# Performance work log

Hardware: AMD Instinct MI355X
Metric: run time of the kernel (lower is better)

## Reference

```python
import jax, jax.numpy as jnp
import numpy as np

N, E, F, R, L, B = 50000, 800000, 64, 20, 2, 64
RC = 5.0
ZMAX = 100
LN2 = 0.6931471805599453

def ssp(x):
    # shifted softplus: softplus(x) - log(2)
    return jax.nn.softplus(x) - LN2

def setup_inputs() -> dict:
    key = jax.random.key(0)
    ks = jax.random.split(key, 32)
    w = lambda i, shape: jax.random.normal(ks[i], shape, dtype=jnp.float32) * 0.05
    inp = {
        'z': jax.random.randint(ks[0], (N,), 0, ZMAX + 1),
        'pos': jax.random.normal(ks[1], (N, 3), dtype=jnp.float32) * 3.0,
        'edge_index': jax.random.randint(ks[2], (2, E), 0, N),
        'batch_idx': jnp.sort(jax.random.randint(ks[3], (N,), 0, B)),
        'emb': jax.random.normal(ks[4], (ZMAX + 1, F), dtype=jnp.float32),
        'phi_W': w(5, (L, 3 * F, F)), 'phi_b': w(6, (L, 3 * F)),
        'filt_W1': w(7, (L, F, R)), 'filt_b1': w(8, (L, F)),
        'filt_W2': w(9, (L, 3 * F, F)), 'filt_b2': w(10, (L, 3 * F)),
        'U_W': w(11, (L, F, F)), 'V_W': w(12, (L, F, F)),
        'a_W1': w(13, (L, F, 2 * F)), 'a_b1': w(14, (L, F)),
        'a_W2': w(15, (L, 3 * F, F)), 'a_b2': w(16, (L, 3 * F)),
        'e_W1': w(17, (F // 2, F)), 'e_b1': w(18, (F // 2,)),
        'e_W2': w(19, (1, F // 2)), 'e_b2': w(20, (1,)),
        'dip_w': w(21, (F,)),
    }
    return inp

def reference(z, pos, edge_index, batch_idx, emb, phi_W, phi_b,
              filt_W1, filt_b1, filt_W2, filt_b2, U_W, V_W,
              a_W1, a_b1, a_W2, a_b2, e_W1, e_b1, e_W2, e_b2, dip_w):
    src, dst = edge_index[0], edge_index[1]
    s = emb[z]                               # (N, F)
    v = jnp.zeros((N, F, 3), dtype=s.dtype)  # (N, F, 3)

    # edge geometry
    r_vec = pos[dst] - pos[src]              # (E, 3)
    r_norm = jnp.linalg.norm(r_vec, axis=-1)
    r_hat = r_vec / jnp.maximum(r_norm, 1e-8)[:, None]
    # Gaussian RBF on [0, RC], widths = grid spacing
    mu = jnp.linspace(0.0, RC, R, dtype=s.dtype)
    width = mu[1] - mu[0]
    e_ij = jnp.exp(-((r_norm[:, None] - mu[None, :]) ** 2) / (2.0 * width * width))
    fc = 0.5 * (jnp.cos(jnp.pi * r_norm / RC) + 1.0) * (r_norm < RC)
    e_ij = e_ij * fc[:, None]                # (E, R)

    for l in range(L):
        # message block
        filt = ssp(e_ij @ filt_W1[l].T + filt_b1[l]) @ filt_W2[l].T + filt_b2[l]  # (E, 3F)
        W_s, W_v, W_r = jnp.split(filt, 3, axis=-1)
        phi = s[dst] @ phi_W[l].T + phi_b[l]                                       # (E, 3F)
        phi_s, phi_v, phi_r = jnp.split(phi, 3, axis=-1)
        m_s = W_s * phi_s                                                          # (E, F)
        m_v = W_v[:, :, None] * v[dst] + (W_r * phi_r)[:, :, None] * r_hat[:, None, :]  # (E, F, 3)
        s = s + jax.ops.segment_sum(m_s, src, num_segments=N)
        v = v + jax.ops.segment_sum(m_v, src, num_segments=N)
        # update block
        Uv = jnp.einsum('nfd,gf->ngd', v, U_W[l])
        Vv = jnp.einsum('nfd,gf->ngd', v, V_W[l])
        Vv_norm_sq = jnp.sum(Vv * Vv, axis=-1)                                     # (N, F)
        a = ssp(jnp.concatenate([s, Vv_norm_sq], axis=-1) @ a_W1[l].T + a_b1[l]) @ a_W2[l].T + a_b2[l]
        a_ss, a_sv, a_vv = jnp.split(a, 3, axis=-1)
        inner = jnp.sum(Uv * Vv, axis=-1)
        s = s + a_ss + a_sv * inner
        v = v + a_vv[:, :, None] * Uv

    # heads
    eps_i = (ssp(s @ e_W1.T + e_b1) @ e_W2.T + e_b2)[:, 0]  # (N,)
    energy = jax.ops.segment_sum(eps_i, batch_idx, num_segments=B)
    mu_i = jnp.sum(v * dip_w[None, :, None], axis=1)         # (N, 3)
    mu_mol = jax.ops.segment_sum(mu_i, batch_idx, num_segments=B)
    dipole = jnp.linalg.norm(mu_mol, axis=-1)
    charges = jnp.zeros((N,), dtype=s.dtype)
    return energy, dipole, charges
```

## Files before the change

kernel.cpp:

```cpp
#include <hip/hip_runtime.h>
#include <math.h>

static constexpr int N  = 50000;
static constexpr int E  = 800000;
static constexpr int F  = 64;
static constexpr int R  = 20;
static constexpr int NL = 2;
static constexpr int B  = 64;
static constexpr float RC   = 5.0f;
static constexpr float LN2F = 0.6931471805599453f;
static constexpr float WIDTH  = RC / (R - 1);
static constexpr float INV2W2 = 1.0f / (2.0f * WIDTH * WIDTH);
static constexpr float PI_F = 3.14159265358979323846f;

static constexpr int   NB     = 4096;
static constexpr float DR     = RC / NB;
static constexpr float INV_DR = NB / RC;
static constexpr int   TROWS  = NB + 2;
static constexpr int   TENT   = NB + 1;

static constexpr int NBLK_SCAN = (N + 255) / 256;

typedef __attribute__((ext_vector_type(8))) short bf16x8;
typedef __attribute__((ext_vector_type(4))) float f32x4;
typedef __attribute__((ext_vector_type(3))) unsigned uint32x3;

__device__ __forceinline__ float ssp_f(float x) {
    return fmaxf(x, 0.0f) + log1pf(__expf(-fabsf(x))) - LN2F;
}

__device__ __forceinline__ short f2bf(float x) {
    unsigned u = __builtin_bit_cast(unsigned, x);
    unsigned r = (u + 0x7fffu + ((u >> 16) & 1u)) >> 16;
    return (short)r;
}
__device__ __forceinline__ float bf_lo(unsigned u) {
    return __builtin_bit_cast(float, u << 16);
}
__device__ __forceinline__ float bf_hi(unsigned u) {
    return __builtin_bit_cast(float, u & 0xffff0000u);
}

__global__ void k_hist(const int* __restrict__ ei, int* __restrict__ cnt) {
    int e = blockIdx.x * blockDim.x + threadIdx.x;
    if (e < E) atomicAdd(&cnt[ei[e]], 1);
}

__global__ void k_scan_a(const int* __restrict__ cnt, int* __restrict__ bsum) {
    __shared__ int part[256];
    const int t = threadIdx.x;
    const int idx = blockIdx.x * 256 + t;
    int v = (idx < N) ? cnt[idx] : 0;
    part[t] = v;
    __syncthreads();
    for (int d = 1; d < 256; d <<= 1) {
        int x = (t >= d) ? part[t - d] : 0;
        __syncthreads();
        part[t] += x;
        __syncthreads();
    }
    if (t == 255) bsum[blockIdx.x] = part[255];
}

__global__ void k_scan_b(const int* __restrict__ bsum, int* __restrict__ bpre,
                         int* __restrict__ offN) {
    __shared__ int part[256];
    const int t = threadIdx.x;
    int v = (t < NBLK_SCAN) ? bsum[t] : 0;
    part[t] = v;
    __syncthreads();
    for (int d = 1; d < 256; d <<= 1) {
        int x = (t >= d) ? part[t - d] : 0;
        __syncthreads();
        part[t] += x;
        __syncthreads();
    }
    if (t < NBLK_SCAN) bpre[t] = part[t] - v;
    if (t == NBLK_SCAN - 1) *offN = part[t];
}

__global__ void k_scan_c(const int* __restrict__ cnt, const int* __restrict__ bpre,
                         int* __restrict__ off, int* __restrict__ curN,
                         int* __restrict__ curF) {
    __shared__ int part[256];
    const int t = threadIdx.x;
    const int idx = blockIdx.x * 256 + t;
    int v = (idx < N) ? cnt[idx] : 0;
    part[t] = v;
    __syncthreads();
    for (int d = 1; d < 256; d <<= 1) {
        int x = (t >= d) ? part[t - d] : 0;
        __syncthreads();
        part[t] += x;
        __syncthreads();
    }
    if (idx < N) {
        int e = bpre[blockIdx.x] + part[t] - v;
        off[idx] = e;
        curN[idx] = e;
        curF[idx] = e + v;
    }
}

__global__ void k_scatter(const int* __restrict__ ei, int* __restrict__ curN,
                          int* __restrict__ curF,
                          const float* __restrict__ pos, uint4* __restrict__ edata) {
    int e = blockIdx.x * blockDim.x + threadIdx.x;
    if (e >= E) return;
    int src = ei[e], dst = ei[E + e];
    float qx = pos[dst * 3 + 0] - pos[src * 3 + 0];
    float qy = pos[dst * 3 + 1] - pos[src * 3 + 1];
    float qz = pos[dst * 3 + 2] - pos[src * 3 + 2];
    float rn = sqrtf(qx * qx + qy * qy + qz * qz);
    float invn = 1.0f / fmaxf(rn, 1e-8f);
    float t = rn * INV_DR;
    int i = (int)t;
    float fr = t - (float)i;
    const bool far = (i >= NB);
    if (far) { i = NB; fr = 0.0f; }
    int p = far ? (atomicAdd(&curF[src], -1) - 1) : atomicAdd(&curN[src], 1);
    uint4 rec;
    rec.x = (unsigned)dst;
    rec.y = (unsigned)i | ((unsigned)(unsigned short)f2bf(fr) << 16);
    rec.z = (unsigned)(unsigned short)f2bf(qx * invn)
          | ((unsigned)(unsigned short)f2bf(qy * invn) << 16);
    rec.w = (unsigned)(unsigned short)f2bf(qz * invn);
    edata[p] = rec;
}

__global__ void k_table(const float* __restrict__ fW1, const float* __restrict__ fb1,
                        const float* __restrict__ fW2, const float* __restrict__ fb2,
                        unsigned short* __restrict__ Tp) {
    const int l   = blockIdx.x / TROWS;
    const int row = blockIdx.x % TROWS;
    const int lane = threadIdx.x;
    const float r = fminf((float)row, (float)NB) * DR;
    const float fc = (r < RC) ? 0.5f * (__cosf(PI_F * r * (1.0f / RC)) + 1.0f) : 0.0f;

    __shared__ float sh[F];
    float acc = fb1[l * F + lane];
    const float* w1 = fW1 + (size_t)l * F * R + (size_t)lane * R;
    #pragma unroll
    for (int rr = 0; rr < R; rr++) {
        float dmu = r - rr * WIDTH;
        float er = __expf(-dmu * dmu * INV2W2) * fc;
        acc = fmaf(er, w1[rr], acc);
    }
    sh[lane] = ssp_f(acc);
    __syncthreads();
    unsigned short* TpL = Tp + (size_t)l * TENT * 384;
    #pragma unroll
    for (int p = 0; p < 3; p++) {
        int c = p * 64 + lane;
        float a = fb2[l * 192 + c];
        const float* w2 = fW2 + ((size_t)l * 192 + c) * 64;
        #pragma unroll 8
        for (int k = 0; k < F; k++) a = fmaf(sh[k], w2[k], a);
        unsigned short bf = (unsigned short)f2bf(a);
        if (row <= NB) TpL[(size_t)row * 384 + lane * 6 + p * 2 + 0] = bf;
        if (row >= 1)  TpL[(size_t)(row - 1) * 384 + lane * 6 + p * 2 + 1] = bf;
    }
}

__launch_bounds__(256)
__global__ void k_pack0(float* __restrict__ s, const int* __restrict__ z,
                        const float* __restrict__ emb,
                        const float* __restrict__ PW, const float* __restrict__ Pb,
                        unsigned* __restrict__ ndA) {
    __shared__ float sbuf[4][F];
    const int lane = threadIdx.x & 63;
    const int wid  = threadIdx.x >> 6;
    const int gwave = blockIdx.x * 4 + wid;
    const int nwaves = gridDim.x * 4;

    float wsr[F], wrr[F];
    {
        const float* rs = PW + (size_t)lane * 64;
        const float* rr = PW + (size_t)(128 + lane) * 64;
        #pragma unroll
        for (int k = 0; k < F; k += 4) {
            float4 a = *(const float4*)(rs + k);
            wsr[k] = a.x; wsr[k+1] = a.y; wsr[k+2] = a.z; wsr[k+3] = a.w;
            float4 b = *(const float4*)(rr + k);
            wrr[k] = b.x; wrr[k+1] = b.y; wrr[k+2] = b.z; wrr[k+3] = b.w;
        }
    }
    const float bs = Pb[lane], br = Pb[128 + lane];

    for (int n = gwave; n < N; n += nwaves) {
        float sv = emb[(size_t)z[n] * F + lane];
        s[(size_t)n * F + lane] = sv;
        sbuf[wid][lane] = sv;
        float as = bs, ar = br;
        #pragma unroll
        for (int k = 0; k < F; k += 4) {
            float4 s4 = *(const float4*)&sbuf[wid][k];
            as = fmaf(s4.x, wsr[k],   as); as = fmaf(s4.y, wsr[k+1], as);
            as = fmaf(s4.z, wsr[k+2], as); as = fmaf(s4.w, wsr[k+3], as);
            ar = fmaf(s4.x, wrr[k],   ar); ar = fmaf(s4.y, wrr[k+1], ar);
            ar = fmaf(s4.z, wrr[k+2], ar); ar = fmaf(s4.w, wrr[k+3], ar);
        }
        ndA[(size_t)n * 64 + lane] = (unsigned)(unsigned short)f2bf(as)
                                   | ((unsigned)(unsigned short)f2bf(ar) << 16);
    }
}

template<bool ACCUMV>
__launch_bounds__(256, 8)
__global__ void k_gather(const uint4* __restrict__ edata, const int* __restrict__ off,
                         const int* __restrict__ mid,
                         const unsigned short* __restrict__ TpL,
                         const unsigned* __restrict__ ndA, const uint2* __restrict__ ndV,
                         float* __restrict__ s, float* __restrict__ v) {
    __shared__ float red[4][4][64];
    const int lane = threadIdx.x & 63;
    const int wv   = threadIdx.x >> 6;
    const int n = blockIdx.x;
    const int base = off[n], m = mid[n], end = off[n + 1];

    float ms = 0.f, mv0 = 0.f, mv1 = 0.f, mv2 = 0.f;

    for (int k = base + wv; k < m; k += 4) {
        const uint4 ed = edata[k];
        const int i = (int)(ed.y & 0xffffu);
        const uint32x3 t = *(const uint32x3*)(TpL + (size_t)i * 384 + lane * 6);
        const unsigned a = ndA[(size_t)ed.x * 64 + lane];
        const float fr = bf_hi(ed.y);
        const float Ws = fmaf(fr, bf_hi(t.x) - bf_lo(t.x), bf_lo(t.x));
        const float Wr = fmaf(fr, bf_hi(t.z) - bf_lo(t.z), bf_lo(t.z));
        ms = fmaf(Ws, bf_lo(a), ms);
        const float c = Wr * bf_hi(a);
        const float rhx = bf_lo(ed.z), rhy = bf_hi(ed.z), rhz = bf_lo(ed.w);
        if (ACCUMV) {
            const float Wv = fmaf(fr, bf_hi(t.y) - bf_lo(t.y), bf_lo(t.y));
            const uint2 w = ndV[(size_t)ed.x * 64 + lane];
            mv0 = fmaf(Wv, bf_lo(w.x), fmaf(c, rhx, mv0));
            mv1 = fmaf(Wv, bf_hi(w.x), fmaf(c, rhy, mv1));
            mv2 = fmaf(Wv, bf_lo(w.y), fmaf(c, rhz, mv2));
        } else {
            mv0 = fmaf(c, rhx, mv0);
            mv1 = fmaf(c, rhy, mv1);
            mv2 = fmaf(c, rhz, mv2);
        }
    }

    {
        const uint32x3 tF = *(const uint32x3*)(TpL + (size_t)NB * 384 + lane * 6);
        const float WsF = bf_lo(tF.x), WvF = bf_lo(tF.y), WrF = bf_lo(tF.z);
        int kc = m + wv;
        if (kc < end) {
            uint4 edC = edata[kc];
            int kn = kc + 4;
            bool hasN = kn < end;
            uint4 edN = edC;
            if (hasN) edN = edata[kn];
            unsigned aC = ndA[(size_t)edC.x * 64 + lane];
            uint2 wC = {0, 0};
            if (ACCUMV) wC = ndV[(size_t)edC.x * 64 + lane];
            for (;;) {
                const int kn2 = kn + 4;
                const bool hasN2 = hasN && (kn2 < end);
                uint4 edN2 = edC;
                if (hasN2) edN2 = edata[kn2];
                unsigned aN = aC;
                uint2 wN = wC;
                if (hasN) {
                    aN = ndA[(size_t)edN.x * 64 + lane];
                    if (ACCUMV) wN = ndV[(size_t)edN.x * 64 + lane];
                }
                ms = fmaf(WsF, bf_lo(aC), ms);
                const float c = WrF * bf_hi(aC);
                const float rhx = bf_lo(edC.z), rhy = bf_hi(edC.z), rhz = bf_lo(edC.w);
                if (ACCUMV) {
                    mv0 = fmaf(WvF, bf_lo(wC.x), fmaf(c, rhx, mv0));
                    mv1 = fmaf(WvF, bf_hi(wC.x), fmaf(c, rhy, mv1));
                    mv2 = fmaf(WvF, bf_lo(wC.y), fmaf(c, rhz, mv2));
                } else {
                    mv0 = fmaf(c, rhx, mv0);
                    mv1 = fmaf(c, rhy, mv1);
                    mv2 = fmaf(c, rhz, mv2);
                }
                if (!hasN) break;
                edC = edN; aC = aN; wC = wN;
                edN = edN2; hasN = hasN2; kn = kn2;
            }
        }
    }

    red[wv][0][lane] = ms;
    red[wv][1][lane] = mv0;
    red[wv][2][lane] = mv1;
    red[wv][3][lane] = mv2;
    __syncthreads();
    if (wv == 0) {
        ms  = red[0][0][lane] + red[1][0][lane] + red[2][0][lane] + red[3][0][lane];
        mv0 = red[0][1][lane] + red[1][1][lane] + red[2][1][lane] + red[3][1][lane];
        mv1 = red[0][2][lane] + red[1][2][lane] + red[2][2][lane] + red[3][2][lane];
        mv2 = red[0][3][lane] + red[1][3][lane] + red[2][3][lane] + red[3][3][lane];
        s[(size_t)n * F + lane] += ms;
        float* vo = v + (size_t)n * 3 * F + lane;
        if (ACCUMV) {
            vo[0]     += mv0;
            vo[F]     += mv1;
            vo[2 * F] += mv2;
        } else {
            vo[0] = mv0; vo[F] = mv1; vo[2 * F] = mv2;
        }
    }
}

__device__ __forceinline__ bf16x8 load_wfrag(const float* __restrict__ Wp, int ldk,
                                             int nrow, int k0) {
    const float* p = Wp + (size_t)nrow * ldk + k0;
    float4 a = *(const float4*)p;
    float4 b = *(const float4*)(p + 4);
    bf16x8 r;
    r[0] = f2bf(a.x); r[1] = f2bf(a.y); r[2] = f2bf(a.z); r[3] = f2bf(a.w);
    r[4] = f2bf(b.x); r[5] = f2bf(b.y); r[6] = f2bf(b.z); r[7] = f2bf(b.w);
    return r;
}

template<bool DO_PACK>
__launch_bounds__(256)
__global__ void k_update_mfma(float* __restrict__ s, float* __restrict__ v,
                              const float* __restrict__ U_W, const float* __restrict__ V_W,
                              const float* __restrict__ aW1, const float* __restrict__ ab1,
                              const float* __restrict__ aW2, const float* __restrict__ ab2,
                              const float* __restrict__ PW, const float* __restrict__ Pb,
                              unsigned* __restrict__ ndA, uint2* __restrict__ ndV) {
    __shared__ short vlds[96 * 72];
    __shared__ short xlds[32 * 136];
    __shared__ short hlds[32 * 72];

    const int tid = threadIdx.x;
    const int l   = tid & 63;
    const int w   = tid >> 6;
    const int lo  = l & 15;
    const int hi  = l >> 4;

    bf16x8 ufr[2], vfr[2], w1fr[4], w2fr[3][2];
    #pragma unroll
    for (int kk = 0; kk < 2; kk++) {
        ufr[kk] = load_wfrag(U_W, 64, w * 16 + lo, kk * 32 + hi * 8);
        vfr[kk] = load_wfrag(V_W, 64, w * 16 + lo, kk * 32 + hi * 8);
    }
    #pragma unroll
    for (int kk = 0; kk < 4; kk++)
        w1fr[kk] = load_wfrag(aW1, 128, w * 16 + lo, kk * 32 + hi * 8);
    #pragma unroll
    for (int p = 0; p < 3; p++)
        #pragma unroll
        for (int kk = 0; kk < 2; kk++)
            w2fr[p][kk] = load_wfrag(aW2, 64, p * 64 + w * 16 + lo, kk * 32 + hi * 8);

    bf16x8 pws[2], pwr[2];
    float pbs = 0.f, pbr = 0.f;
    if (DO_PACK) {
        #pragma unroll
        for (int kk = 0; kk < 2; kk++) {
            pws[kk] = load_wfrag(PW, 64, w * 16 + lo, kk * 32 + hi * 8);
            pwr[kk] = load_wfrag(PW, 64, 128 + w * 16 + lo, kk * 32 + hi * 8);
        }
        pbs = Pb[w * 16 + lo];
        pbr = Pb[128 + w * 16 + lo];
    }

    const float ab1c  = ab1[w * 16 + lo];
    const float ab2c0 = ab2[w * 16 + lo];
    const float ab2c1 = ab2[64 + w * 16 + lo];
    const float ab2c2 = ab2[128 + w * 16 + lo];
    const int g = w * 16 + lo;

    for (int half = 0; half < 2; half++) {
        const int n0 = blockIdx.x * 64 + half * 32;
        if (half) __syncthreads();

        for (int u = tid; u < 96 * 8; u += 256) {
            int row = u >> 3, oct = u & 7;
            int d = row >> 5, nn = row & 31;
            int n = min(n0 + nn, N - 1);
            const float* src = v + ((size_t)n * 3 + d) * 64 + oct * 8;
            float4 a = *(const float4*)src;
            float4 b = *(const float4*)(src + 4);
            bf16x8 t;
            t[0] = f2bf(a.x); t[1] = f2bf(a.y); t[2] = f2bf(a.z); t[3] = f2bf(a.w);
            t[4] = f2bf(b.x); t[5] = f2bf(b.y); t[6] = f2bf(b.z); t[7] = f2bf(b.w);
            *(bf16x8*)&vlds[row * 72 + oct * 8] = t;
        }
        for (int u = tid; u < 32 * 8; u += 256) {
            int nn = u >> 3, oct = u & 7;
            int n = min(n0 + nn, N - 1);
            const float* src = s + (size_t)n * 64 + oct * 8;
            float4 a = *(const float4*)src;
            float4 b = *(const float4*)(src + 4);
            bf16x8 t;
            t[0] = f2bf(a.x); t[1] = f2bf(a.y); t[2] = f2bf(a.z); t[3] = f2bf(a.w);
            t[4] = f2bf(b.x); t[5] = f2bf(b.y); t[6] = f2bf(b.z); t[7] = f2bf(b.w);
            *(bf16x8*)&xlds[nn * 136 + oct * 8] = t;
        }
        __syncthreads();

        f32x4 cu[6], cv[6];
        #pragma unroll
        for (int mt = 0; mt < 6; mt++) { cu[mt] = (f32x4)0.0f; cv[mt] = (f32x4)0.0f; }
        #pragma unroll
        for (int kk = 0; kk < 2; kk++) {
            #pragma unroll
            for (int mt = 0; mt < 6; mt++) {
                bf16x8 af = *(const bf16x8*)&vlds[(mt * 16 + lo) * 72 + kk * 32 + hi * 8];
                cu[mt] = __builtin_amdgcn_mfma_f32_16x16x32_bf16(af, ufr[kk], cu[mt], 0, 0, 0);
                cv[mt] = __builtin_amdgcn_mfma_f32_16x16x32_bf16(af, vfr[kk], cv[mt], 0, 0, 0);
            }
        }

        f32x4 inn[2];
        #pragma unroll
        for (int nt = 0; nt < 2; nt++) {
            #pragma unroll
            for (int r = 0; r < 4; r++) {
                float vs = 0.f, ii = 0.f;
                #pragma unroll
                for (int d = 0; d < 3; d++) {
                    float a = cu[d * 2 + nt][r], b = cv[d * 2 + nt][r];
                    vs = fmaf(b, b, vs);
                    ii = fmaf(a, b, ii);
                }
                inn[nt][r] = ii;
                int nl = nt * 16 + hi * 4 + r;
                xlds[nl * 136 + 64 + w * 16 + lo] = f2bf(vs);
            }
        }
        __syncthreads();

        f32x4 c2[2];
        c2[0] = (f32x4)0.0f; c2[1] = (f32x4)0.0f;
        #pragma unroll
        for (int kk = 0; kk < 4; kk++) {
            #pragma unroll
            for (int mt = 0; mt < 2; mt++) {
                bf16x8 af = *(const bf16x8*)&xlds[(mt * 16 + lo) * 136 + kk * 32 + hi * 8];
                c2[mt] = __builtin_amdgcn_mfma_f32_16x16x32_bf16(af, w1fr[kk], c2[mt], 0, 0, 0);
            }
        }
        #pragma unroll
        for (int mt = 0; mt < 2; mt++)
            #pragma unroll
            for (int r = 0; r < 4; r++) {
                float hv = ssp_f(c2[mt][r] + ab1c);
                hlds[(mt * 16 + hi * 4 + r) * 72 + w * 16 + lo] = f2bf(hv);
            }
        __syncthreads();

        f32x4 c3[2][3];
        #pragma unroll
        for (int mt = 0; mt < 2; mt++)
            #pragma unroll
            for (int p = 0; p < 3; p++) c3[mt][p] = (f32x4)0.0f;
        #pragma unroll
        for (int kk = 0; kk < 2; kk++) {
            #pragma unroll
            for (int mt = 0; mt < 2; mt++) {
                bf16x8 af = *(const bf16x8*)&hlds[(mt * 16 + lo) * 72 + kk * 32 + hi * 8];
                #pragma unroll
                for (int p = 0; p < 3; p++)
                    c3[mt][p] = __builtin_amdgcn_mfma_f32_16x16x32_bf16(af, w2fr[p][kk], c3[mt][p], 0, 0, 0);
            }
        }

        float snew[2][4];
        #pragma unroll
        for (int mt = 0; mt < 2; mt++) {
            #pragma unroll
            for (int r = 0; r < 4; r++) {
                int n = n0 + mt * 16 + hi * 4 + r;
                if (n >= N) { snew[mt][r] = 0.f; continue; }
                float a_ss = c3[mt][0][r] + ab2c0;
                float a_sv = c3[mt][1][r] + ab2c1;
                float a_vv = c3[mt][2][r] + ab2c2;
                size_t si = (size_t)n * 64 + g;
                float sn = s[si] + a_ss + a_sv * inn[mt][r];
                s[si] = sn;
                snew[mt][r] = sn;
                float vn[3];
                #pragma unroll
                for (int d = 0; d < 3; d++) {
                    size_t vi = ((size_t)n * 3 + d) * 64 + g;
                    vn[d] = v[vi] + a_vv * cu[d * 2 + mt][r];
                    v[vi] = vn[d];
                }
                if (DO_PACK) {
                    uint2 pv;
                    pv.x = (unsigned)(unsigned short)f2bf(vn[0])
                         | ((unsigned)(unsigned short)f2bf(vn[1]) << 16);
                    pv.y = (unsigned)(unsigned short)f2bf(vn[2]);
                    ndV[(size_t)n * 64 + g] = pv;
                }
            }
        }

        if (DO_PACK) {
            __syncthreads();
            #pragma unroll
            for (int mt = 0; mt < 2; mt++)
                #pragma unroll
                for (int r = 0; r < 4; r++)
                    hlds[(mt * 16 + hi * 4 + r) * 72 + g] = f2bf(snew[mt][r]);
            __syncthreads();

            f32x4 cs[2], cr[2];
            cs[0] = (f32x4)0.0f; cs[1] = (f32x4)0.0f;
            cr[0] = (f32x4)0.0f; cr[1] = (f32x4)0.0f;
            #pragma unroll
            for (int kk = 0; kk < 2; kk++) {
                #pragma unroll
                for (int mt = 0; mt < 2; mt++) {
                    bf16x8 af = *(const bf16x8*)&hlds[(mt * 16 + lo) * 72 + kk * 32 + hi * 8];
                    cs[mt] = __builtin_amdgcn_mfma_f32_16x16x32_bf16(af, pws[kk], cs[mt], 0, 0, 0);
                    cr[mt] = __builtin_amdgcn_mfma_f32_16x16x32_bf16(af, pwr[kk], cr[mt], 0, 0, 0);
                }
            }
            #pragma unroll
            for (int mt = 0; mt < 2; mt++) {
                #pragma unroll
                for (int r = 0; r < 4; r++) {
                    int n = n0 + mt * 16 + hi * 4 + r;
                    if (n >= N) continue;
                    ndA[(size_t)n * 64 + g] =
                          (unsigned)(unsigned short)f2bf(cs[mt][r] + pbs)
                        | ((unsigned)(unsigned short)f2bf(cr[mt][r] + pbr) << 16);
                }
            }
        }
    }
}

__global__ void k_heads(const float* __restrict__ s, const float* __restrict__ v,
                        const int* __restrict__ batch_idx,
                        const float* __restrict__ eW1, const float* __restrict__ eb1,
                        const float* __restrict__ eW2, const float* __restrict__ eb2,
                        const float* __restrict__ dip_w,
                        float* __restrict__ eacc, float* __restrict__ macc) {
    __shared__ float se[B];
    __shared__ float sm[3][B];
    if (threadIdx.x < B) se[threadIdx.x] = 0.0f;
    if (threadIdx.x < 3 * B) sm[threadIdx.x >> 6][threadIdx.x & 63] = 0.0f;
    __syncthreads();
    int n = blockIdx.x * blockDim.x + threadIdx.x;
    if (n < N) {
        int b = batch_idx[n];
        float sr[F];
        #pragma unroll
        for (int f = 0; f < F; f += 4) {
            float4 t = *(const float4*)&s[(size_t)n * F + f];
            sr[f] = t.x; sr[f+1] = t.y; sr[f+2] = t.z; sr[f+3] = t.w;
        }
        float eps = eb2[0];
        for (int jj = 0; jj < F / 2; jj++) {
            float acc = eb1[jj];
            #pragma unroll
            for (int f = 0; f < F; f++)
                acc = fmaf(sr[f], eW1[jj * F + f], acc);
            eps = fmaf(eW2[jj], ssp_f(acc), eps);
        }
        atomicAdd(&se[b], eps);
        #pragma unroll
        for (int d = 0; d < 3; d++) {
            float m = 0.0f;
            #pragma unroll 8
            for (int f = 0; f < F; f++)
                m = fmaf(v[((size_t)n * 3 + d) * F + f], dip_w[f], m);
            atomicAdd(&sm[d][b], m);
        }
    }
    __syncthreads();
    if (threadIdx.x < B) atomicAdd(&eacc[threadIdx.x], se[threadIdx.x]);
    if (threadIdx.x >= B && threadIdx.x < 4 * B) {
        int d = (threadIdx.x >> 6) - 1, b = threadIdx.x & 63;
        atomicAdd(&macc[d * B + b], sm[d][b]);
    }
}

__global__ void k_final(const float* __restrict__ eacc, const float* __restrict__ macc,
                        float* __restrict__ out) {
    int b = threadIdx.x;
    if (b < B) {
        out[b] = eacc[b];
        float mx = macc[b], my = macc[B + b], mz = macc[2 * B + b];
        out[B + b] = sqrtf(mx * mx + my * my + mz * mz);
    }
}

extern "C" void kernel_launch(void* const* d_in, const int* in_sizes, int n_in,
                              void* d_out, int out_size, void* d_ws, size_t ws_size,
                              hipStream_t stream) {
    const int*   z     = (const int*)d_in[0];
    const float* pos   = (const float*)d_in[1];
    const int*   ei    = (const int*)d_in[2];
    const int*   bidx  = (const int*)d_in[3];
    const float* emb   = (const float*)d_in[4];
    const float* phi_W = (const float*)d_in[5];
    const float* phi_b = (const float*)d_in[6];
    const float* fW1   = (const float*)d_in[7];
    const float* fb1   = (const float*)d_in[8];
    const float* fW2   = (const float*)d_in[9];
    const float* fb2   = (const float*)d_in[10];
    const float* U_W   = (const float*)d_in[11];
    const float* V_W   = (const float*)d_in[12];
    const float* aW1   = (const float*)d_in[13];
    const float* ab1   = (const float*)d_in[14];
    const float* aW2   = (const float*)d_in[15];
    const float* ab2   = (const float*)d_in[16];
    const float* eW1   = (const float*)d_in[17];
    const float* eb1   = (const float*)d_in[18];
    const float* eW2   = (const float*)d_in[19];
    const float* eb2   = (const float*)d_in[20];
    const float* dip_w = (const float*)d_in[21];
    float* out = (float*)d_out;

    float* ws = (float*)d_ws;
    float* s    = ws;
    float* v    = s + (size_t)N * F;
    unsigned* ndA = (unsigned*)(v + (size_t)N * F * 3);
    uint2* ndV  = (uint2*)(ndA + (size_t)N * 64);
    unsigned short* Tp = (unsigned short*)(ndV + (size_t)N * 64);
    float* eacc = (float*)(Tp + (size_t)NL * TENT * 384);
    float* macc = eacc + B;
    int*   cnt  = (int*)(macc + 3 * B);
    int*   off  = cnt  + N;
    int*   curN = off  + N + 1;
    int*   curF = curN + N;
    int*   bsum = curF + N;
    int*   bpre = bsum + 256;
    uint4* edata = (uint4*)(((uintptr_t)(bpre + 256) + 15) & ~(uintptr_t)15);

    hipMemsetAsync(cnt,  0, sizeof(int) * N, stream);
    hipMemsetAsync(eacc, 0, sizeof(float) * 4 * B, stream);
    hipMemsetAsync(out + 2 * B, 0, sizeof(float) * (size_t)N, stream);

    k_hist<<<(E + 255) / 256, 256, 0, stream>>>(ei, cnt);
    k_scan_a<<<NBLK_SCAN, 256, 0, stream>>>(cnt, bsum);
    k_scan_b<<<1, 256, 0, stream>>>(bsum, bpre, off + N);
    k_scan_c<<<NBLK_SCAN, 256, 0, stream>>>(cnt, bpre, off, curN, curF);
    k_scatter<<<(E + 255) / 256, 256, 0, stream>>>(ei, curN, curF, pos, edata);
    k_table<<<NL * TROWS, 64, 0, stream>>>(fW1, fb1, fW2, fb2, Tp);

    const int ublocks = (N + 63) / 64;
    k_pack0<<<512, 256, 0, stream>>>(s, z, emb, phi_W, phi_b, ndA);
    k_gather<false><<<N, 256, 0, stream>>>(edata, off, curN, Tp, ndA, ndV, s, v);
    k_update_mfma<true><<<ublocks, 256, 0, stream>>>(s, v,
        U_W, V_W, aW1, ab1, aW2, ab2,
        phi_W + (size_t)192 * 64, phi_b + 192, ndA, ndV);
    k_gather<true><<<N, 256, 0, stream>>>(edata, off, curN,
        Tp + (size_t)TENT * 384, ndA, ndV, s, v);
    k_update_mfma<false><<<ublocks, 256, 0, stream>>>(s, v,
        U_W + 4096, V_W + 4096, aW1 + 8192, ab1 + F, aW2 + 12288, ab2 + 192,
        nullptr, nullptr, nullptr, nullptr);

    k_heads<<<(N + 255) / 256, 256, 0, stream>>>(s, v, bidx, eW1, eb1, eW2, eb2,
                                                 dip_w, eacc, macc);
    k_final<<<1, 64, 0, stream>>>(eacc, macc, out);
}
```

Measured before the change: 527.9 us.

## Assign one wave per node in gather and interleave node A/V packs

The gather kernel now maps each node to a single wave, four nodes per block, instead of splitting one node's edges across four waves. This removes the shared-memory reduction and the block barrier. The loop now handles near and far edges in one software-pipelined loop that prefetches the table row. The separate ndA and ndV node arrays are merged into one 12-byte-per-lane interleaved array, so the second-layer gather issues a single 12-byte load per neighbor instead of two loads. High-degree nodes now run serially on one wave, which may raise per-node latency and cause load imbalance.

```diff
diff --git a/kernel.cpp b/kernel.cpp
--- a/kernel.cpp
+++ b/kernel.cpp
@@ -166,7 +166,7 @@
 __global__ void k_pack0(float* __restrict__ s, const int* __restrict__ z,
                         const float* __restrict__ emb,
                         const float* __restrict__ PW, const float* __restrict__ Pb,
-                        unsigned* __restrict__ ndA) {
+                        unsigned* __restrict__ ndA0) {
     __shared__ float sbuf[4][F];
     const int lane = threadIdx.x & 63;
     const int wid  = threadIdx.x >> 6;
@@ -200,8 +200,8 @@
             ar = fmaf(s4.x, wrr[k],   ar); ar = fmaf(s4.y, wrr[k+1], ar);
             ar = fmaf(s4.z, wrr[k+2], ar); ar = fmaf(s4.w, wrr[k+3], ar);
         }
-        ndA[(size_t)n * 64 + lane] = (unsigned)(unsigned short)f2bf(as)
-                                   | ((unsigned)(unsigned short)f2bf(ar) << 16);
+        ndA0[(size_t)n * 64 + lane] = (unsigned)(unsigned short)f2bf(as)
+                                    | ((unsigned)(unsigned short)f2bf(ar) << 16);
     }
 }
 
@@ -210,102 +210,81 @@
 __global__ void k_gather(const uint4* __restrict__ edata, const int* __restrict__ off,
                          const int* __restrict__ mid,
                          const unsigned short* __restrict__ TpL,
-                         const unsigned* __restrict__ ndA, const uint2* __restrict__ ndV,
+                         const unsigned* __restrict__ ndA0,
+                         const unsigned* __restrict__ ndAV,
                          float* __restrict__ s, float* __restrict__ v) {
-    __shared__ float red[4][4][64];
     const int lane = threadIdx.x & 63;
     const int wv   = threadIdx.x >> 6;
-    const int n = blockIdx.x;
+    const int n = blockIdx.x * 4 + wv;
+    if (n >= N) return;
     const int base = off[n], m = mid[n], end = off[n + 1];
 
+    const uint32x3 tFar = *(const uint32x3*)(TpL + (size_t)NB * 384 + lane * 6);
+
     float ms = 0.f, mv0 = 0.f, mv1 = 0.f, mv2 = 0.f;
 
-    for (int k = base + wv; k < m; k += 4) {
-        const uint4 ed = edata[k];
-        const int i = (int)(ed.y & 0xffffu);
-        const uint32x3 t = *(const uint32x3*)(TpL + (size_t)i * 384 + lane * 6);
-        const unsigned a = ndA[(size_t)ed.x * 64 + lane];
-        const float fr = bf_hi(ed.y);
-        const float Ws = fmaf(fr, bf_hi(t.x) - bf_lo(t.x), bf_lo(t.x));
-        const float Wr = fmaf(fr, bf_hi(t.z) - bf_lo(t.z), bf_lo(t.z));
-        ms = fmaf(Ws, bf_lo(a), ms);
-        const float c = Wr * bf_hi(a);
-        const float rhx = bf_lo(ed.z), rhy = bf_hi(ed.z), rhz = bf_lo(ed.w);
+    if (base < end) {
+        uint4 edC = edata[base];
+        int kn = base + 1;
+        bool hasN = kn < end;
+        uint4 edN = edC;
+        if (hasN) edN = edata[kn];
+        uint32x3 tC = tFar;
+        if (base < m)
+            tC = *(const uint32x3*)(TpL + (size_t)(edC.y & 0xffffu) * 384 + lane * 6);
+        uint32x3 rC;
         if (ACCUMV) {
-            const float Wv = fmaf(fr, bf_hi(t.y) - bf_lo(t.y), bf_lo(t.y));
-            const uint2 w = ndV[(size_t)ed.x * 64 + lane];
-            mv0 = fmaf(Wv, bf_lo(w.x), fmaf(c, rhx, mv0));
-            mv1 = fmaf(Wv, bf_hi(w.x), fmaf(c, rhy, mv1));
-            mv2 = fmaf(Wv, bf_lo(w.y), fmaf(c, rhz, mv2));
+            rC = *(const uint32x3*)(ndAV + ((size_t)edC.x * 64 + lane) * 3);
         } else {
-            mv0 = fmaf(c, rhx, mv0);
-            mv1 = fmaf(c, rhy, mv1);
-            mv2 = fmaf(c, rhz, mv2);
-        }
-    }
-
-    {
-        const uint32x3 tF = *(const uint32x3*)(TpL + (size_t)NB * 384 + lane * 6);
-        const float WsF = bf_lo(tF.x), WvF = bf_lo(tF.y), WrF = bf_lo(tF.z);
-        int kc = m + wv;
-        if (kc < end) {
-            uint4 edC = edata[kc];
-            int kn = kc + 4;
-            bool hasN = kn < end;
-            uint4 edN = edC;
-            if (hasN) edN = edata[kn];
-            unsigned aC = ndA[(size_t)edC.x * 64 + lane];
-            uint2 wC = {0, 0};
-            if (ACCUMV) wC = ndV[(size_t)edC.x * 64 + lane];
-            for (;;) {
-                const int kn2 = kn + 4;
-                const bool hasN2 = hasN && (kn2 < end);
-                uint4 edN2 = edC;
-                if (hasN2) edN2 = edata[kn2];
-                unsigned aN = aC;
-                uint2 wN = wC;
-                if (hasN) {
-                    aN = ndA[(size_t)edN.x * 64 + lane];
-                    if (ACCUMV) wN = ndV[(size_t)edN.x * 64 + lane];
+            rC.x = ndA0[(size_t)edC.x * 64 + lane]; rC.y = 0; rC.z = 0;
+        }
+
+        for (;;) {
+            const int kn2 = kn + 1;
+            const bool hasN2 = hasN && (kn2 < end);
+            uint4 edN2 = edC;
+            if (hasN2) edN2 = edata[kn2];
+            uint32x3 tN = tC, rN = rC;
+            if (hasN) {
+                tN = tFar;
+                if (kn < m)
+                    tN = *(const uint32x3*)(TpL + (size_t)(edN.y & 0xffffu) * 384 + lane * 6);
+                if (ACCUMV) {
+                    rN = *(const uint32x3*)(ndAV + ((size_t)edN.x * 64 + lane) * 3);
+                } else {
+                    rN.x = ndA0[(size_t)edN.x * 64 + lane];
                 }
-                ms = fmaf(WsF, bf_lo(aC), ms);
-                const float c = WrF * bf_hi(aC);
-                const float rhx = bf_lo(edC.z), rhy = bf_hi(edC.z), rhz = bf_lo(edC.w);
-                if (ACCUMV) {
-                    mv0 = fmaf(WvF, bf_lo(wC.x), fmaf(c, rhx, mv0));
-                    mv1 = fmaf(WvF, bf_hi(wC.x), fmaf(c, rhy, mv1));
-                    mv2 = fmaf(WvF, bf_lo(wC.y), fmaf(c, rhz, mv2));
-                } else {
-                    mv0 = fmaf(c, rhx, mv0);
-                    mv1 = fmaf(c, rhy, mv1);
-                    mv2 = fmaf(c, rhz, mv2);
-                }
-                if (!hasN) break;
-                edC = edN; aC = aN; wC = wN;
-                edN = edN2; hasN = hasN2; kn = kn2;
-            }
-        }
-    }
-
-    red[wv][0][lane] = ms;
-    red[wv][1][lane] = mv0;
-    red[wv][2][lane] = mv1;
-    red[wv][3][lane] = mv2;
-    __syncthreads();
-    if (wv == 0) {
-        ms  = red[0][0][lane] + red[1][0][lane] + red[2][0][lane] + red[3][0][lane];
-        mv0 = red[0][1][lane] + red[1][1][lane] + red[2][1][lane] + red[3][1][lane];
-        mv1 = red[0][2][lane] + red[1][2][lane] + red[2][2][lane] + red[3][2][lane];
-        mv2 = red[0][3][lane] + red[1][3][lane] + red[2][3][lane] + red[3][3][lane];
-        s[(size_t)n * F + lane] += ms;
-        float* vo = v + (size_t)n * 3 * F + lane;
-        if (ACCUMV) {
-            vo[0]     += mv0;
-            vo[F]     += mv1;
-            vo[2 * F] += mv2;
-        } else {
-            vo[0] = mv0; vo[F] = mv1; vo[2 * F] = mv2;
-        }
+            }
+            const float fr = bf_hi(edC.y);
+            const float Ws = fmaf(fr, bf_hi(tC.x) - bf_lo(tC.x), bf_lo(tC.x));
+            const float Wr = fmaf(fr, bf_hi(tC.z) - bf_lo(tC.z), bf_lo(tC.z));
+            ms = fmaf(Ws, bf_lo(rC.x), ms);
+            const float c = Wr * bf_hi(rC.x);
+            const float rhx = bf_lo(edC.z), rhy = bf_hi(edC.z), rhz = bf_lo(edC.w);
+            if (ACCUMV) {
+                const float Wv = fmaf(fr, bf_hi(tC.y) - bf_lo(tC.y), bf_lo(tC.y));
+                mv0 = fmaf(Wv, bf_lo(rC.y), fmaf(c, rhx, mv0));
+                mv1 = fmaf(Wv, bf_hi(rC.y), fmaf(c, rhy, mv1));
+                mv2 = fmaf(Wv, bf_lo(rC.z), fmaf(c, rhz, mv2));
+            } else {
+                mv0 = fmaf(c, rhx, mv0);
+                mv1 = fmaf(c, rhy, mv1);
+                mv2 = fmaf(c, rhz, mv2);
+            }
+            if (!hasN) break;
+            edC = edN; tC = tN; rC = rN;
+            edN = edN2; hasN = hasN2; kn = kn2;
+        }
+    }
+
+    s[(size_t)n * F + lane] += ms;
+    float* vo = v + (size_t)n * 3 * F + lane;
+    if (ACCUMV) {
+        vo[0]     += mv0;
+        vo[F]     += mv1;
+        vo[2 * F] += mv2;
+    } else {
+        vo[0] = mv0; vo[F] = mv1; vo[2 * F] = mv2;
     }
 }
 
@@ -327,7 +306,7 @@
                               const float* __restrict__ aW1, const float* __restrict__ ab1,
                               const float* __restrict__ aW2, const float* __restrict__ ab2,
                               const float* __restrict__ PW, const float* __restrict__ Pb,
-                              unsigned* __restrict__ ndA, uint2* __restrict__ ndV) {
+                              unsigned* __restrict__ ndAV) {
     __shared__ short vlds[96 * 72];
     __shared__ short xlds[32 * 136];
     __shared__ short hlds[32 * 72];
@@ -489,11 +468,10 @@
                     v[vi] = vn[d];
                 }
                 if (DO_PACK) {
-                    uint2 pv;
-                    pv.x = (unsigned)(unsigned short)f2bf(vn[0])
-                         | ((unsigned)(unsigned short)f2bf(vn[1]) << 16);
-                    pv.y = (unsigned)(unsigned short)f2bf(vn[2]);
-                    ndV[(size_t)n * 64 + g] = pv;
+                    unsigned* pp = ndAV + ((size_t)n * 64 + g) * 3;
+                    pp[1] = (unsigned)(unsigned short)f2bf(vn[0])
+                          | ((unsigned)(unsigned short)f2bf(vn[1]) << 16);
+                    pp[2] = (unsigned)(unsigned short)f2bf(vn[2]);
                 }
             }
         }
@@ -525,7 +503,7 @@
                 for (int r = 0; r < 4; r++) {
                     int n = n0 + mt * 16 + hi * 4 + r;
                     if (n >= N) continue;
-                    ndA[(size_t)n * 64 + g] =
+                    ndAV[((size_t)n * 64 + g) * 3] =
                           (unsigned)(unsigned short)f2bf(cs[mt][r] + pbs)
                         | ((unsigned)(unsigned short)f2bf(cr[mt][r] + pbr) << 16);
                 }
@@ -620,9 +598,9 @@
     float* ws = (float*)d_ws;
     float* s    = ws;
     float* v    = s + (size_t)N * F;
-    unsigned* ndA = (unsigned*)(v + (size_t)N * F * 3);
-    uint2* ndV  = (uint2*)(ndA + (size_t)N * 64);
-    unsigned short* Tp = (unsigned short*)(ndV + (size_t)N * 64);
+    unsigned* ndA0 = (unsigned*)(v + (size_t)N * F * 3);
+    unsigned* ndAV = ndA0 + (size_t)N * 64;
+    unsigned short* Tp = (unsigned short*)(ndAV + (size_t)N * 64 * 3);
     float* eacc = (float*)(Tp + (size_t)NL * TENT * 384);
     float* macc = eacc + B;
     int*   cnt  = (int*)(macc + 3 * B);
@@ -644,17 +622,18 @@
     k_scatter<<<(E + 255) / 256, 256, 0, stream>>>(ei, curN, curF, pos, edata);
     k_table<<<NL * TROWS, 64, 0, stream>>>(fW1, fb1, fW2, fb2, Tp);
 
+    const int gblocks = (N + 3) / 4;
     const int ublocks = (N + 63) / 64;
-    k_pack0<<<512, 256, 0, stream>>>(s, z, emb, phi_W, phi_b, ndA);
-    k_gather<false><<<N, 256, 0, stream>>>(edata, off, curN, Tp, ndA, ndV, s, v);
+    k_pack0<<<512, 256, 0, stream>>>(s, z, emb, phi_W, phi_b, ndA0);
+    k_gather<false><<<gblocks, 256, 0, stream>>>(edata, off, curN, Tp, ndA0, ndAV, s, v);
     k_update_mfma<true><<<ublocks, 256, 0, stream>>>(s, v,
         U_W, V_W, aW1, ab1, aW2, ab2,
-        phi_W + (size_t)192 * 64, phi_b + 192, ndA, ndV);
-    k_gather<true><<<N, 256, 0, stream>>>(edata, off, curN,
-        Tp + (size_t)TENT * 384, ndA, ndV, s, v);
+        phi_W + (size_t)192 * 64, phi_b + 192, ndAV);
+    k_gather<true><<<gblocks, 256, 0, stream>>>(edata, off, curN,
+        Tp + (size_t)TENT * 384, ndA0, ndAV, s, v);
     k_update_mfma<false><<<ublocks, 256, 0, stream>>>(s, v,
         U_W + 4096, V_W + 4096, aW1 + 8192, ab1 + F, aW2 + 12288, ab2 + 192,
-        nullptr, nullptr, nullptr, nullptr);
+        nullptr, nullptr, nullptr);
 
     k_heads<<<(N + 255) / 256, 256, 0, stream>>>(s, v, bidx, eW1, eb1, eW2, eb2,
                                                  dip_w, eacc, macc);
```

New measurement: 528.8 us. No clear change (+0.2%).
